# Performance work log

Measured on AMD Instinct MI355X. Metric: run time of the kernel, lower is better.

## Reference

```python
import jax, jax.numpy as jnp
import numpy as np

K = 7       # kernel_size (window is K x K, padding=(K-1)//2, stride=1)
HEADS = 4   # number of heads; mid_channels = C // HEADS


def _unfold(x, k):
    # Emulates nn.Unfold(k, padding=(k-1)//2, stride=1) followed by reshape to
    # (B, C, P, H, W) with P = k*k ordered as (ki, kj) per channel (torch order).
    B, C, H, W = x.shape
    p = (k - 1) // 2
    xp = jnp.pad(x, ((0, 0), (0, 0), (p, p), (p, p)))  # zeros padding_mode
    patches = [xp[:, :, i:i + H, j:j + W] for i in range(k) for j in range(k)]
    return jnp.stack(patches, axis=2)  # (B, C, P, H, W)


def setup_inputs() -> dict:
    key = jax.random.key(0)
    x = jax.random.normal(key, (4, 64, 128, 128), dtype=jnp.float32)
    return {"x": x}


def reference(x):
    B, C, H, W = x.shape
    mid = C // HEADS
    P = K * K
    # (B, heads, mid, P, H, W)
    x_unf = _unfold(x, K).reshape(B, HEADS, mid, P, H, W)
    x_r = x.reshape(B, HEADS, mid, H, W)
    # squared L2 distance between center pixel feature and each window patch pixel
    A = ((x_unf ** 2).sum(axis=2)
         + (x_r ** 2).sum(axis=2, keepdims=True)
         - 2.0 * jnp.einsum('bgcphw,bgchw->bgphw', x_unf, x_r))  # (B,G,P,H,W)
    A = jax.nn.softmax(-A, axis=2)
    y = jnp.einsum('bgphw,bgcphw->bgchw', A, x_unf).reshape(B, C, H, W)
    return x + y  # residual=True
```

## Files before the change

kernel.cpp:

```cpp
#include <hip/hip_runtime.h>


#define TW    16
#define RAD   3
#define HWD   22
#define NPIX  (HWD * HWD)
#define MID   16
#define PSTRD 10
#define IMG   128
#define PLANE (IMG * IMG)

__device__ __forceinline__ unsigned bf16rne(float v) {
    unsigned u = __float_as_uint(v);
    u += 0x7fffu + ((u >> 16) & 1u);
    return u >> 16;
}
__device__ __forceinline__ float bl(unsigned u) { return __uint_as_float(u << 16); }
__device__ __forceinline__ float bh(unsigned u) { return __uint_as_float(u & 0xffff0000u); }

__device__ __forceinline__ float xor1_sum(float v) {
    int o = __builtin_amdgcn_update_dpp(0, __float_as_int(v),
                                        0xB1 ,
                                        0xF, 0xF, true);
    return v + __int_as_float(o);
}

__global__ __launch_bounds__(512)
void nlm_kernel(const float* __restrict__ x, float* __restrict__ out) {
    const int g   = blockIdx.z & 3;
    const int b   = blockIdx.z >> 2;
    const int tx0 = blockIdx.x * TW;
    const int ty0 = blockIdx.y * TW;

    __shared__ __align__(8) unsigned recd[NPIX * PSTRD];

    const int tid  = threadIdx.x;
    const int half = tid & 1;
    const int pix  = tid >> 1;
    const int lx   = pix & 15;
    const int ly   = pix >> 4;
    const float* xb = x + (size_t)(b * 64 + g * MID) * PLANE;

    if (tid < NPIX) {
        const int yy = tid / HWD;
        const int xx = tid - yy * HWD;
        const int gy = ty0 + yy - RAD;
        const int gx = tx0 + xx - RAD;
        const bool in = ((unsigned)gy < (unsigned)IMG) & ((unsigned)gx < (unsigned)IMG);
        const float* p = xb + gy * IMG + gx;
        unsigned pk[8];
        float ss = 0.f;
        #pragma unroll
        for (int k = 0; k < 8; ++k) {
            const float v0 = in ? p[(2 * k) * PLANE] : 0.f;
            const float v1 = in ? p[(2 * k + 1) * PLANE] : 0.f;
            const unsigned q0 = bf16rne(v0);
            const unsigned q1 = bf16rne(v1);
            pk[k] = q0 | (q1 << 16);
            const float r0 = __uint_as_float(q0 << 16);
            const float r1 = __uint_as_float(q1 << 16);
            ss = fmaf(r0, r0, ss);
            ss = fmaf(r1, r1, ss);
        }
        unsigned* rp = &recd[tid * PSTRD];
        #pragma unroll
        for (int k = 0; k < 4; ++k)
            *reinterpret_cast<uint2*>(rp + 2 * k) = make_uint2(pk[2 * k], pk[2 * k + 1]);
        rp[8] = __float_as_uint(ss);
    }
    __syncthreads();

    const float* cp = xb + (size_t)(half * 8) * PLANE + (ty0 + ly) * IMG + (tx0 + lx);
    float ctr[8];
    #pragma unroll
    for (int c = 0; c < 8; ++c) ctr[c] = cp[c * PLANE];
    float cch = 0.f;
    #pragma unroll
    for (int c = 0; c < 8; ++c) cch = fmaf(ctr[c], ctr[c], cch);
    const float cc = xor1_sum(cch);

    float acc[8];
    #pragma unroll
    for (int c = 0; c < 8; ++c) acc[c] = 0.f;
    float s = 0.f;

    #pragma unroll 1
    for (int wy = 0; wy < 7; ++wy) {
        const unsigned* rp = &recd[((ly + wy) * HWD + lx) * PSTRD + 4 * half];
        #pragma unroll 1
        for (int wx = 0; wx < 7; ++wx) {
            const uint2 q0 = *reinterpret_cast<const uint2*>(rp + 0);
            const uint2 q1 = *reinterpret_cast<const uint2*>(rp + 2);
            const float nn = __uint_as_float(rp[8 - 4 * half]);
            float nb[8];
            nb[0] = bl(q0.x); nb[1] = bh(q0.x);
            nb[2] = bl(q0.y); nb[3] = bh(q0.y);
            nb[4] = bl(q1.x); nb[5] = bh(q1.x);
            nb[6] = bl(q1.y); nb[7] = bh(q1.y);
            float d0 = 0.f, d1 = 0.f;
            #pragma unroll
            for (int c = 0; c < 8; c += 2) {
                d0 = fmaf(nb[c + 0], ctr[c + 0], d0);
                d1 = fmaf(nb[c + 1], ctr[c + 1], d1);
            }
            const float dot = xor1_sum(d0 + d1);
            const float w = __expf(fmaf(2.f, dot, -(nn + cc)));
            s += w;
            #pragma unroll
            for (int c = 0; c < 8; ++c) acc[c] = fmaf(w, nb[c], acc[c]);
            rp += PSTRD;
        }
    }

    const float inv = 1.f / s;
    float* ob = out + (size_t)(b * 64 + g * MID + half * 8) * PLANE
                    + (size_t)(ty0 + ly) * IMG + (tx0 + lx);
    #pragma unroll
    for (int c = 0; c < 8; ++c)
        ob[c * PLANE] = fmaf(acc[c], inv, ctr[c]);
}

extern "C" void kernel_launch(void* const* d_in, const int* in_sizes, int n_in,
                              void* d_out, int out_size, void* d_ws, size_t ws_size,
                              hipStream_t stream) {
    const float* x = (const float*)d_in[0];
    float* out = (float*)d_out;
    dim3 grid(IMG / TW, IMG / TW, 16);
    nlm_kernel<<<grid, 512, 0, stream>>>(x, out);
}
```

Before: 32.60 us.

## Split window rows between thread pair instead of channels, reduce at end

```diff
diff --git a/kernel.cpp b/kernel.cpp
--- a/kernel.cpp
+++ b/kernel.cpp
@@ -6,9 +6,10 @@
 #define HWD   22
 #define NPIX  (HWD * HWD)
 #define MID   16
-#define PSTRD 10
+#define PSTRD 12
 #define IMG   128
 #define PLANE (IMG * IMG)
+#define LOG2E 1.4426950408889634f
 
 __device__ __forceinline__ unsigned bf16rne(float v) {
     unsigned u = __float_as_uint(v);
@@ -32,13 +33,9 @@
     const int tx0 = blockIdx.x * TW;
     const int ty0 = blockIdx.y * TW;
 
-    __shared__ __align__(8) unsigned recd[NPIX * PSTRD];
+    __shared__ __align__(16) unsigned recd[NPIX * PSTRD];
 
-    const int tid  = threadIdx.x;
-    const int half = tid & 1;
-    const int pix  = tid >> 1;
-    const int lx   = pix & 15;
-    const int ly   = pix >> 4;
+    const int tid = threadIdx.x;
     const float* xb = x + (size_t)(b * 64 + g * MID) * PLANE;
 
     if (tid < NPIX) {
@@ -63,61 +60,79 @@
             ss = fmaf(r1, r1, ss);
         }
         unsigned* rp = &recd[tid * PSTRD];
-        #pragma unroll
-        for (int k = 0; k < 4; ++k)
-            *reinterpret_cast<uint2*>(rp + 2 * k) = make_uint2(pk[2 * k], pk[2 * k + 1]);
-        rp[8] = __float_as_uint(ss);
+        *reinterpret_cast<uint4*>(rp + 0) = make_uint4(pk[0], pk[1], pk[2], pk[3]);
+        *reinterpret_cast<uint4*>(rp + 4) = make_uint4(pk[4], pk[5], pk[6], pk[7]);
+        rp[8] = __float_as_uint(ss * LOG2E);
     }
     __syncthreads();
 
-    const float* cp = xb + (size_t)(half * 8) * PLANE + (ty0 + ly) * IMG + (tx0 + lx);
-    float ctr[8];
+    const int h   = tid & 1;
+    const int pix = tid >> 1;
+    const int lx  = pix & 15;
+    const int ly  = pix >> 4;
+
+    const float* cp = xb + (ty0 + ly) * IMG + (tx0 + lx);
+    float ctr[MID];
     #pragma unroll
-    for (int c = 0; c < 8; ++c) ctr[c] = cp[c * PLANE];
-    float cch = 0.f;
+    for (int c = 0; c < MID; ++c) ctr[c] = cp[c * PLANE];
+    float c0 = 0.f, c1 = 0.f;
     #pragma unroll
-    for (int c = 0; c < 8; ++c) cch = fmaf(ctr[c], ctr[c], cch);
-    const float cc = xor1_sum(cch);
+    for (int c = 0; c < MID; c += 2) {
+        c0 = fmaf(ctr[c], ctr[c], c0);
+        c1 = fmaf(ctr[c + 1], ctr[c + 1], c1);
+    }
+    const float ccL = (c0 + c1) * LOG2E;
 
-    float acc[8];
+    float acc[MID];
     #pragma unroll
-    for (int c = 0; c < 8; ++c) acc[c] = 0.f;
+    for (int c = 0; c < MID; ++c) acc[c] = 0.f;
     float s = 0.f;
 
     #pragma unroll 1
-    for (int wy = 0; wy < 7; ++wy) {
-        const unsigned* rp = &recd[((ly + wy) * HWD + lx) * PSTRD + 4 * half];
+    for (int wy = h; wy < 7; wy += 2) {
+        const unsigned* rp = &recd[((ly + wy) * HWD + lx) * PSTRD];
         #pragma unroll 1
         for (int wx = 0; wx < 7; ++wx) {
-            const uint2 q0 = *reinterpret_cast<const uint2*>(rp + 0);
-            const uint2 q1 = *reinterpret_cast<const uint2*>(rp + 2);
-            const float nn = __uint_as_float(rp[8 - 4 * half]);
-            float nb[8];
-            nb[0] = bl(q0.x); nb[1] = bh(q0.x);
-            nb[2] = bl(q0.y); nb[3] = bh(q0.y);
-            nb[4] = bl(q1.x); nb[5] = bh(q1.x);
-            nb[6] = bl(q1.y); nb[7] = bh(q1.y);
-            float d0 = 0.f, d1 = 0.f;
+            const uint4 q0 = *reinterpret_cast<const uint4*>(rp + 0);
+            const uint4 q1 = *reinterpret_cast<const uint4*>(rp + 4);
+            const float nnL = __uint_as_float(rp[8]);
+            float nb[MID];
+            nb[0]  = bl(q0.x); nb[1]  = bh(q0.x);
+            nb[2]  = bl(q0.y); nb[3]  = bh(q0.y);
+            nb[4]  = bl(q0.z); nb[5]  = bh(q0.z);
+            nb[6]  = bl(q0.w); nb[7]  = bh(q0.w);
+            nb[8]  = bl(q1.x); nb[9]  = bh(q1.x);
+            nb[10] = bl(q1.y); nb[11] = bh(q1.y);
+            nb[12] = bl(q1.z); nb[13] = bh(q1.z);
+            nb[14] = bl(q1.w); nb[15] = bh(q1.w);
+
+            float d0 = 0.f, d1 = 0.f, d2 = 0.f, d3 = 0.f;
             #pragma unroll
-            for (int c = 0; c < 8; c += 2) {
+            for (int c = 0; c < MID; c += 4) {
                 d0 = fmaf(nb[c + 0], ctr[c + 0], d0);
                 d1 = fmaf(nb[c + 1], ctr[c + 1], d1);
+                d2 = fmaf(nb[c + 2], ctr[c + 2], d2);
+                d3 = fmaf(nb[c + 3], ctr[c + 3], d3);
             }
-            const float dot = xor1_sum(d0 + d1);
-            const float w = __expf(fmaf(2.f, dot, -(nn + cc)));
+            const float dot = (d0 + d1) + (d2 + d3);
+            const float w = exp2f(fmaf(2.f * LOG2E, dot, -(nnL + ccL)));
             s += w;
             #pragma unroll
-            for (int c = 0; c < 8; ++c) acc[c] = fmaf(w, nb[c], acc[c]);
+            for (int c = 0; c < MID; ++c) acc[c] = fmaf(w, nb[c], acc[c]);
             rp += PSTRD;
         }
     }
 
+    s = xor1_sum(s);
+    #pragma unroll
+    for (int c = 0; c < MID; ++c) acc[c] = xor1_sum(acc[c]);
+
     const float inv = 1.f / s;
-    float* ob = out + (size_t)(b * 64 + g * MID + half * 8) * PLANE
+    float* ob = out + (size_t)(b * 64 + g * MID + 8 * h) * PLANE
                     + (size_t)(ty0 + ly) * IMG + (tx0 + lx);
     #pragma unroll
     for (int c = 0; c < 8; ++c)
-        ob[c * PLANE] = fmaf(acc[c], inv, ctr[c]);
+        ob[c * PLANE] = fmaf(acc[8 * h + c], inv, ctr[8 * h + c]);
 }
 
 extern "C" void kernel_launch(void* const* d_in, const int* in_sizes, int n_in,
```

New measurement: 44.50 us. 36.5% more time.
